# Kernel tuning notes

Measured on AMD Instinct MI355X. Metric: run time of the kernel, lower is better.

## Reference

```python
import jax, jax.numpy as jnp
import numpy as np

NC = 80          # num classes
REG_MAX = 16     # DFL bins
STRIDES = (8, 16, 32)
FEAT_HW = ((80, 80), (40, 40), (20, 20))
MAX_DET = 100
CONF_THRES = 0.25
IOU_THRES = 0.45
PRE_TOPK = 1000  # pre-NMS candidate count (EfficientNMS-style preselection)


def setup_inputs() -> dict:
    key = jax.random.key(0)
    k1, k2, k3 = jax.random.split(key, 3)
    B = 32
    no = 4 * REG_MAX + NC  # 144
    return {
        "p3": jax.random.normal(k1, (B, no, 80, 80), dtype=jnp.float32),
        "p4": jax.random.normal(k2, (B, no, 40, 40), dtype=jnp.float32),
        "p5": jax.random.normal(k3, (B, no, 20, 20), dtype=jnp.float32),
    }


def _make_anchors():
    # grid_cell_offset = 0.5, matching ultralytics make_anchors
    pts, strs = [], []
    for (h, w), s in zip(FEAT_HW, STRIDES):
        sx = jnp.arange(w, dtype=jnp.float32) + 0.5
        sy = jnp.arange(h, dtype=jnp.float32) + 0.5
        yy, xx = jnp.meshgrid(sy, sx, indexing="ij")
        pts.append(jnp.stack([xx.ravel(), yy.ravel()], axis=-1))  # [h*w, 2]
        strs.append(jnp.full((h * w, 1), float(s), dtype=jnp.float32))
    return jnp.concatenate(pts, 0), jnp.concatenate(strs, 0)  # [A,2], [A,1]


def _pairwise_iou(b):
    # b: [K, 4] xyxy
    area = (b[:, 2] - b[:, 0]) * (b[:, 3] - b[:, 1])
    lt = jnp.maximum(b[:, None, :2], b[None, :, :2])
    rb = jnp.minimum(b[:, None, 2:], b[None, :, 2:])
    wh = jnp.clip(rb - lt, 0.0)
    inter = wh[..., 0] * wh[..., 1]
    return inter / (area[:, None] + area[None, :] - inter + 1e-7)


def _nms_single(bxyxy, conf):
    # Greedy class-agnostic NMS over PRE_TOPK score-sorted boxes.
    K = bxyxy.shape[0]
    iou = _pairwise_iou(bxyxy)  # [K, K]
    idx = jnp.arange(K)

    def step(suppressed, xs):
        i, row = xs
        keep = jnp.logical_and(jnp.logical_not(suppressed[i]), conf[i] > 0.0)
        suppressed = jnp.logical_or(suppressed, keep & (row > IOU_THRES) & (idx > i))
        return suppressed, keep

    _, keeps = jax.lax.scan(step, jnp.zeros(K, dtype=bool), (idx, iou))
    return keeps  # [K] bool


def reference(p3, p4, p5):
    feats = [p3, p4, p5]
    B = p3.shape[0]
    no = 4 * REG_MAX + NC
    # concat across scales: [B, no, A]
    x_cat = jnp.concatenate([f.reshape(B, no, -1) for f in feats], axis=2)
    box, cls = x_cat[:, : 4 * REG_MAX], x_cat[:, 4 * REG_MAX:]

    anchors, strd = _make_anchors()  # [A,2], [A,1]
    A = box.shape[-1]

    # DFL: softmax over reg_max bins, expectation with arange weights
    prob = jax.nn.softmax(box.reshape(B, 4, REG_MAX, A), axis=2)
    dist = jnp.einsum("bkra,r->bka", prob, jnp.arange(REG_MAX, dtype=jnp.float32))

    # dist2bbox (xywh) then scale by stride
    anc = anchors.T  # [2, A]
    lt, rb = dist[:, :2], dist[:, 2:]
    x1y1 = anc - lt
    x2y2 = anc + rb
    dbox = jnp.concatenate([(x1y1 + x2y2) * 0.5, x2y2 - x1y1], axis=1) * strd.T  # [B,4,A]

    boxes = dbox.transpose(0, 2, 1)                       # [B, A, 4] xywh
    scores = jax.nn.sigmoid(cls).transpose(0, 2, 1)       # [B, A, NC] (score_activation=1)

    # class-agnostic: best class per box
    conf = scores.max(-1)                                 # [B, A]
    cls_id = jnp.argmax(scores, -1)                       # [B, A]
    conf_m = jnp.where(conf > CONF_THRES, conf, -1.0)

    topv, topi = jax.lax.top_k(conf_m, PRE_TOPK)          # [B, K]
    bsel = jnp.take_along_axis(boxes, topi[..., None], axis=1)  # [B, K, 4]
    cx, cy, w, h = bsel[..., 0], bsel[..., 1], bsel[..., 2], bsel[..., 3]
    bxyxy = jnp.stack([cx - w * 0.5, cy - h * 0.5, cx + w * 0.5, cy + h * 0.5], -1)

    keeps = jax.vmap(_nms_single)(bxyxy, topv)            # [B, K]
    kept_scores = jnp.where(keeps, topv, -1.0)
    dv, di = jax.lax.top_k(kept_scores, MAX_DET)          # [B, MAX_DET]
    valid = dv > 0.0

    det_scores = jnp.where(valid, dv, 0.0)
    det_boxes = jnp.take_along_axis(bxyxy, di[..., None], axis=1) * valid[..., None]
    sel_cls = jnp.take_along_axis(jnp.take_along_axis(cls_id, topi, 1), di, 1)
    det_classes = jnp.where(valid, sel_cls, 0).astype(jnp.int32)
    num_dets = valid.sum(-1, keepdims=True).astype(jnp.int32)
    return num_dets, det_boxes, det_scores, det_classes
```

## Files before the change

### kernel.cpp

```cpp
#include <hip/hip_runtime.h>
#include <math.h>

#define NCLS 80
#define NA 8400
#define NB 32
#define NO 144
#define PRE_TOPK 1000
#define MAX_DET 100

template<int HW, int WDIM, int S>
__device__ __forceinline__ void decode_blk(
    const float* __restrict__ src, int b, int a0, int aoff,
    float* __restrict__ conf, int* __restrict__ clsid, float* __restrict__ box,
    float* s_tile)
{
    int t = threadIdx.x;
    int w = t >> 6;
    int l = t & 63;

    {
        int ch_base = w * 36;
        int chl = ch_base + (l >> 4);
        int aq = (l & 15) * 4;
        int aqc = a0 + aq; if (aqc > HW - 4) aqc = HW - 4;
        const float* gsrc = src + ((size_t)b * NO) * HW + aqc;
        float4 stg[9];
        #pragma unroll
        for (int i = 0; i < 9; ++i)
            stg[i] = *(const float4*)(gsrc + (size_t)(chl + i * 4) * HW);
        #pragma unroll
        for (int i = 0; i < 9; ++i)
            *(float4*)&s_tile[(chl + i * 4) * 64 + aq] = stg[i];
    }
    __syncthreads();

    float v[16];
    #pragma unroll
    for (int r = 0; r < 16; ++r) v[r] = s_tile[(w * 16 + r) * 64 + l];
    float mm = v[0];
    #pragma unroll
    for (int r = 1; r < 16; ++r) mm = fmaxf(mm, v[r]);
    float sum = 0.f, d = 0.f;
    #pragma unroll
    for (int r = 0; r < 16; ++r) {
        float e = __expf(v[r] - mm);
        sum += e;
        d += e * (float)r;
    }
    d *= 1.0f / sum;

    float c[20];
    #pragma unroll
    for (int cc = 0; cc < 20; ++cc) c[cc] = s_tile[(64 + w * 20 + cc) * 64 + l];
    float m = c[0]; int ii = 0;
    #pragma unroll
    for (int cc = 1; cc < 20; ++cc) if (c[cc] > m) { m = c[cc]; ii = cc; }

    __syncthreads();

    float* s_dfl = s_tile;
    float* s_mx  = s_tile + 320;
    int*   s_id  = (int*)(s_tile + 640);
    s_dfl[l * 5 + w] = d;
    s_mx[l * 5 + w]  = m;
    s_id[l * 5 + w]  = w * 20 + ii;
    __syncthreads();

    if (t < 64 && a0 + t < HW) {
        int pos2 = a0 + t;
        float d0 = s_dfl[t * 5 + 0], d1 = s_dfl[t * 5 + 1];
        float d2 = s_dfl[t * 5 + 2], d3 = s_dfl[t * 5 + 3];
        float bm = s_mx[t * 5 + 0]; int bid = s_id[t * 5 + 0];
        float m1 = s_mx[t * 5 + 1]; if (m1 > bm) { bm = m1; bid = s_id[t * 5 + 1]; }
        float m2 = s_mx[t * 5 + 2]; if (m2 > bm) { bm = m2; bid = s_id[t * 5 + 2]; }
        float m3 = s_mx[t * 5 + 3]; if (m3 > bm) { bm = m3; bid = s_id[t * 5 + 3]; }
        float conf_v = 1.0f / (1.0f + __expf(-bm));

        float ax = (float)(pos2 % WDIM) + 0.5f;
        float ay = (float)(pos2 / WDIM) + 0.5f;
        float x1 = ax - d0, y1 = ay - d1;
        float x2 = ax + d2, y2 = ay + d3;
        float cx = ((x1 + x2) * 0.5f) * (float)S;
        float cy = ((y1 + y2) * 0.5f) * (float)S;
        float ww = (x2 - x1) * (float)S;
        float hh = (y2 - y1) * (float)S;

        size_t gid = (size_t)b * NA + aoff + pos2;
        conf[gid]  = conf_v;
        clsid[gid] = bid;
        *(float4*)(box + gid * 4) = make_float4(cx, cy, ww, hh);
    }
}

__global__ __launch_bounds__(256) void k_decode(
    const float* __restrict__ p3, const float* __restrict__ p4, const float* __restrict__ p5,
    float* __restrict__ conf, int* __restrict__ clsid, float* __restrict__ box)
{
    __shared__ float s_tile[NO * 64];
    int blk = blockIdx.x;
    int b = blk / 132;
    int r = blk - b * 132;
    if (r < 100)       decode_blk<6400, 80, 8>(p3, b, r * 64, 0, conf, clsid, box, s_tile);
    else if (r < 125)  decode_blk<1600, 40, 16>(p4, b, (r - 100) * 64, 6400, conf, clsid, box, s_tile);
    else               decode_blk<400, 20, 32>(p5, b, (r - 125) * 64, 8000, conf, clsid, box, s_tile);
}

__device__ __forceinline__ uint32_t ord_bits(float f) {
    uint32_t u = __float_as_uint(f);
    return (u & 0x80000000u) ? ~u : (u | 0x80000000u);
}

__global__ __launch_bounds__(1024) void k_select(
    const float* __restrict__ conf, const float* __restrict__ box, const int* __restrict__ clsid,
    float* __restrict__ topv, float* __restrict__ bxyxy, int* __restrict__ topcls)
{
    int b = blockIdx.x;
    int t = threadIdx.x;
    int lane = t & 63;

    __shared__ uint32_t ob[NA];
    __shared__ uint32_t hist[256];
    __shared__ uint64_t sbuf[1024];
    __shared__ uint32_t s_prefix;
    __shared__ int s_k;
    __shared__ int s_cnt;

    const float* cf = conf + (size_t)b * NA;
    for (int i = t; i < NA; i += 1024) {
        float c = cf[i];
        float cm = (c > 0.25f) ? c : -1.0f;
        ob[i] = ord_bits(cm);
    }
    if (t == 0) { s_prefix = 0; s_k = PRE_TOPK; s_cnt = 0; }
    sbuf[t] = 0;
    __syncthreads();

    for (int pass = 0; pass < 4; ++pass) {
        int shift = 24 - 8 * pass;
        if (t < 256) hist[t] = 0;
        __syncthreads();
        uint32_t prefix = s_prefix;
        int k = s_k;
        for (int i = t; i < NA; i += 1024) {
            uint32_t key = ob[i];
            bool match = (pass == 0) || (((key ^ prefix) >> (32 - 8 * pass)) == 0);
            uint32_t d = (key >> shift) & 255u;
            if (match) {
                uint64_t m = __ballot(1);
                #pragma unroll
                for (int bb = 0; bb < 8; ++bb) {
                    uint64_t bal = __ballot((d >> bb) & 1u);
                    m &= ((d >> bb) & 1u) ? bal : ~bal;
                }
                if ((m & ((1ull << lane) - 1ull)) == 0ull)
                    atomicAdd(&hist[d], (uint32_t)__popcll(m));
            }
        }
        __syncthreads();
        if (t < 64) {
            uint32_t h0 = hist[4 * t + 0], h1 = hist[4 * t + 1];
            uint32_t h2 = hist[4 * t + 2], h3 = hist[4 * t + 3];
            uint32_t part = h0 + h1 + h2 + h3;
            uint32_t s = part;
            #pragma unroll
            for (int off = 1; off < 64; off <<= 1) {
                uint32_t v = __shfl_down(s, off);
                if (t + off < 64) s += v;
            }
            uint32_t cb3 = s - part;
            uint32_t cb2 = cb3 + h3;
            uint32_t cb1 = cb2 + h2;
            uint32_t cb0 = cb1 + h1;
            uint32_t ku = (uint32_t)k;
            if (cb3 < ku && ku <= cb3 + h3) { s_k = k - (int)cb3; s_prefix = prefix | ((uint32_t)(4 * t + 3) << shift); }
            if (cb2 < ku && ku <= cb2 + h2) { s_k = k - (int)cb2; s_prefix = prefix | ((uint32_t)(4 * t + 2) << shift); }
            if (cb1 < ku && ku <= cb1 + h1) { s_k = k - (int)cb1; s_prefix = prefix | ((uint32_t)(4 * t + 1) << shift); }
            if (cb0 < ku && ku <= cb0 + h0) { s_k = k - (int)cb0; s_prefix = prefix | ((uint32_t)(4 * t + 0) << shift); }
        }
        __syncthreads();
    }

    uint32_t kstar = s_prefix;
    for (int i = t; i < NA; i += 1024) {
        uint32_t key = ob[i];
        if (key >= kstar) {
            int p = atomicAdd(&s_cnt, 1);
            if (p < 1024) sbuf[p] = ((uint64_t)key << 14) | (uint64_t)(16383 - i);
        }
    }
    __syncthreads();

    uint64_t v = sbuf[t];
    for (int k = 2; k <= 1024; k <<= 1) {
        for (int j = k >> 1; j > 0; j >>= 1) {
            uint64_t o;
            if (j >= 64) {
                sbuf[t] = v;
                __syncthreads();
                o = sbuf[t ^ j];
                __syncthreads();
            } else {
                o = __shfl_xor((unsigned long long)v, j);
            }
            bool desc  = ((t & k) == 0);
            bool lower = ((t & j) == 0);
            v = (desc == lower) ? (v > o ? v : o) : (v < o ? v : o);
        }
    }

    if (t < PRE_TOPK) {
        uint64_t key = v;
        uint32_t u = (uint32_t)(key >> 14);
        uint32_t fb = (u & 0x80000000u) ? (u ^ 0x80000000u) : ~u;
        float val = __uint_as_float(fb);
        int idx = 16383 - (int)(key & 16383u);
        size_t g = (size_t)b * NA + idx;
        float4 bx = *(const float4*)(box + g * 4);
        float cx = bx.x, cy = bx.y, w = bx.z, h = bx.w;
        size_t o = (size_t)b * PRE_TOPK + t;
        topv[o] = val;
        *(float4*)(bxyxy + o * 4) = make_float4(cx - w * 0.5f, cy - h * 0.5f,
                                                cx + w * 0.5f, cy + h * 0.5f);
        topcls[o] = clsid[g];
    }
}

__device__ __forceinline__ int bslot(int j) { return j + (j >> 6); }

__global__ __launch_bounds__(256) void k_iou(
    const float* __restrict__ bxyxy, unsigned long long* __restrict__ mask)
{
    __shared__ float4 boxes[PRE_TOPK + 16];
    int b = blockIdx.y;
    int t = threadIdx.x;
    const float4* bp = (const float4*)(bxyxy + (size_t)b * PRE_TOPK * 4);
    for (int i = t; i < PRE_TOPK; i += 256) boxes[bslot(i)] = bp[i];
    __syncthreads();

    int r_local = t >> 4, w = t & 15;
    int row = blockIdx.x * 16 + r_local;
    if (row >= PRE_TOPK) return;

    float4 bi = boxes[bslot(row)];
    float area_i = (bi.z - bi.x) * (bi.w - bi.y);
    unsigned long long bits = 0;
    int j0 = w * 64;
    #pragma unroll 4
    for (int jj = 0; jj < 64; ++jj) {
        int j = j0 + jj;
        if (j >= PRE_TOPK) break;
        if (j <= row) continue;
        float4 bj = boxes[bslot(j)];
        float lx = fmaxf(bi.x, bj.x), ly = fmaxf(bi.y, bj.y);
        float rx = fminf(bi.z, bj.z), ry = fminf(bi.w, bj.w);
        float iw = fmaxf(rx - lx, 0.f), ih = fmaxf(ry - ly, 0.f);
        float inter = iw * ih;
        float area_j = (bj.z - bj.x) * (bj.w - bj.y);
        float iou = inter / (area_i + area_j - inter + 1e-7f);
        if (iou > 0.45f) bits |= (1ull << jj);
    }
    mask[((size_t)b * PRE_TOPK + row) * 16 + w] = bits;
}

__global__ __launch_bounds__(1024) void k_nms(
    const unsigned long long* __restrict__ mask, const float* __restrict__ topv,
    const float* __restrict__ bxyxy, const int* __restrict__ topcls,
    float* __restrict__ out)
{
    int b = blockIdx.x;
    int t = threadIdx.x;

    __shared__ __align__(16) unsigned long long smask[PRE_TOPK * 16];
    __shared__ float sv[PRE_TOPK];
    __shared__ unsigned long long s_valid[16];
    __shared__ int kept[MAX_DET];
    __shared__ int s_cnt;

    for (int i = t; i < PRE_TOPK; i += 1024) sv[i] = topv[(size_t)b * PRE_TOPK + i];
    {
        const ulonglong2* src = (const ulonglong2*)(mask + (size_t)b * PRE_TOPK * 16);
        ulonglong2* dst = (ulonglong2*)smask;
        for (int i = t; i < PRE_TOPK * 8; i += 1024) dst[i] = src[i];
    }
    __syncthreads();

    {
        bool pred = (t < PRE_TOPK) && (sv[t] > 0.0f);
        unsigned long long bal = __ballot(pred);
        if ((t & 63) == 0) s_valid[t >> 6] = bal;
    }
    __syncthreads();

    if (t < 64) {
        int w = t;
        unsigned long long supp = 0;
        unsigned long long valid = (w < 16) ? s_valid[w] : 0ull;
        int base = w * 64;
        int cur = -1;
        int cnt = 0;
        while (cnt < MAX_DET) {
            unsigned long long gt;
            if (cur < base)            gt = ~0ull;
            else if (cur - base >= 63) gt = 0ull;
            else                       gt = (~0ull) << (cur - base + 1);
            unsigned long long cand = valid & ~supp & gt;
            int idx = cand ? (base + __builtin_ctzll(cand)) : 0x7FFFFFFF;
            #pragma unroll
            for (int off = 8; off >= 1; off >>= 1) {
                int o = __shfl_xor(idx, off);
                idx = (o < idx) ? o : idx;
            }
            int nxt = __shfl(idx, 0);
            if (nxt == 0x7FFFFFFF) break;
            if (t == 0) kept[cnt] = nxt;
            ++cnt;
            if (w < 16) supp |= smask[nxt * 16 + w];
            cur = nxt;
        }
        if (t == 0) s_cnt = cnt;
    }
    __syncthreads();

    int cnt = s_cnt; if (cnt > MAX_DET) cnt = MAX_DET;
    if (t == 0) out[b] = (float)cnt;
    if (t < MAX_DET) {
        bool valid = t < cnt;
        float bx0 = 0.f, bx1 = 0.f, bx2 = 0.f, bx3 = 0.f, sc = 0.f, cl = 0.f;
        if (valid) {
            int p = kept[t];
            size_t o = (size_t)b * PRE_TOPK + p;
            float4 bb = *(const float4*)(bxyxy + o * 4);
            bx0 = bb.x; bx1 = bb.y; bx2 = bb.z; bx3 = bb.w;
            sc = sv[p];
            cl = (float)topcls[o];
        }
        size_t db = 32 + ((size_t)b * MAX_DET + t) * 4;
        out[db + 0] = bx0; out[db + 1] = bx1; out[db + 2] = bx2; out[db + 3] = bx3;
        out[32 + 12800 + (size_t)b * MAX_DET + t] = sc;
        out[32 + 16000 + (size_t)b * MAX_DET + t] = cl;
    }
}

extern "C" void kernel_launch(void* const* d_in, const int* in_sizes, int n_in,
                              void* d_out, int out_size, void* d_ws, size_t ws_size,
                              hipStream_t stream)
{
    const float* p3 = (const float*)d_in[0];
    const float* p4 = (const float*)d_in[1];
    const float* p5 = (const float*)d_in[2];
    float* out = (float*)d_out;

    char* ws = (char*)d_ws;
    size_t off_mask = 0;
    size_t off_conf = off_mask + (size_t)NB * PRE_TOPK * 16 * 8;
    size_t off_cls  = off_conf + (size_t)NB * NA * 4;
    size_t off_box  = off_cls  + (size_t)NB * NA * 4;
    size_t off_topv = off_box  + (size_t)NB * NA * 4 * 4;
    size_t off_topc = off_topv + (size_t)NB * PRE_TOPK * 4;
    size_t off_bx   = off_topc + (size_t)NB * PRE_TOPK * 4;

    unsigned long long* mask = (unsigned long long*)(ws + off_mask);
    float* conf   = (float*)(ws + off_conf);
    int*   clsid  = (int*)(ws + off_cls);
    float* box    = (float*)(ws + off_box);
    float* topv   = (float*)(ws + off_topv);
    int*   topcls = (int*)(ws + off_topc);
    float* bxyxy  = (float*)(ws + off_bx);

    k_decode<<<NB * 132, 256, 0, stream>>>(p3, p4, p5, conf, clsid, box);
    k_select<<<NB, 1024, 0, stream>>>(conf, box, clsid, topv, bxyxy, topcls);
    k_iou<<<dim3((PRE_TOPK + 15) / 16, NB), 256, 0, stream>>>(bxyxy, mask);
    k_nms<<<NB, 1024, 0, stream>>>(mask, topv, bxyxy, topcls, out);
}
```

Measured before the change: 136.4 us.

## Merge select, IoU and NMS kernels into one cooperative kernel with grid syncs

Replaces the three post-decode kernels with a single cooperative kernel of 128 blocks. It runs top-k selection on 32 blocks, the IoU mask on all blocks via a strided task loop, and greedy NMS on 32 blocks, separated by grid-wide syncs. The goal is to remove two kernel launch gaps. In exchange, the IoU stage runs on 128 blocks instead of about 2000 small ones, each block reloads boxes per task, and grid syncs add their own cost.

```diff
diff --git a/kernel.cpp b/kernel.cpp
--- a/kernel.cpp
+++ b/kernel.cpp
@@ -1,5 +1,8 @@
 #include <hip/hip_runtime.h>
+#include <hip/hip_cooperative_groups.h>
 #include <math.h>
+
+namespace cg = cooperative_groups;
 
 #define NCLS 80
 #define NA 8400
@@ -7,6 +10,7 @@
 #define NO 144
 #define PRE_TOPK 1000
 #define MAX_DET 100
+#define POST_GRID 128
 
 template<int HW, int WDIM, int S>
 __device__ __forceinline__ void decode_blk(
@@ -105,239 +109,247 @@
     else               decode_blk<400, 20, 32>(p5, b, (r - 125) * 64, 8000, conf, clsid, box, s_tile);
 }
 
+#define SMX 132416
+
+__device__ __forceinline__ int bslot(int j) { return j + (j >> 6); }
+
 __device__ __forceinline__ uint32_t ord_bits(float f) {
     uint32_t u = __float_as_uint(f);
     return (u & 0x80000000u) ? ~u : (u | 0x80000000u);
 }
 
-__global__ __launch_bounds__(1024) void k_select(
+__global__ __launch_bounds__(1024) void k_post(
     const float* __restrict__ conf, const float* __restrict__ box, const int* __restrict__ clsid,
-    float* __restrict__ topv, float* __restrict__ bxyxy, int* __restrict__ topcls)
+    float* __restrict__ topv, float* __restrict__ bxyxy, int* __restrict__ topcls,
+    unsigned long long* __restrict__ mask, float* __restrict__ out)
 {
-    int b = blockIdx.x;
+    cg::grid_group grid = cg::this_grid();
     int t = threadIdx.x;
     int lane = t & 63;
 
-    __shared__ uint32_t ob[NA];
-    __shared__ uint32_t hist[256];
-    __shared__ uint64_t sbuf[1024];
+    __shared__ __align__(16) char smem[SMX];
     __shared__ uint32_t s_prefix;
     __shared__ int s_k;
-    __shared__ int s_cnt;
-
-    const float* cf = conf + (size_t)b * NA;
-    for (int i = t; i < NA; i += 1024) {
-        float c = cf[i];
-        float cm = (c > 0.25f) ? c : -1.0f;
-        ob[i] = ord_bits(cm);
-    }
-    if (t == 0) { s_prefix = 0; s_k = PRE_TOPK; s_cnt = 0; }
-    sbuf[t] = 0;
-    __syncthreads();
-
-    for (int pass = 0; pass < 4; ++pass) {
-        int shift = 24 - 8 * pass;
-        if (t < 256) hist[t] = 0;
-        __syncthreads();
-        uint32_t prefix = s_prefix;
-        int k = s_k;
+    __shared__ int s_cmp_cnt;
+    __shared__ unsigned long long s_valid[16];
+    __shared__ int s_nms_cnt;
+
+    if (blockIdx.x < NB) {
+        int b = blockIdx.x;
+        uint32_t* ob   = (uint32_t*)smem;
+        uint32_t* hist = (uint32_t*)(smem + 33600);
+        uint64_t* sbuf = (uint64_t*)(smem + 34624);
+
+        const float* cf = conf + (size_t)b * NA;
+        for (int i = t; i < NA; i += 1024) {
+            float c = cf[i];
+            float cm = (c > 0.25f) ? c : -1.0f;
+            ob[i] = ord_bits(cm);
+        }
+        if (t == 0) { s_prefix = 0; s_k = PRE_TOPK; s_cmp_cnt = 0; }
+        sbuf[t] = 0;
+        __syncthreads();
+
+        for (int pass = 0; pass < 4; ++pass) {
+            int shift = 24 - 8 * pass;
+            if (t < 256) hist[t] = 0;
+            __syncthreads();
+            uint32_t prefix = s_prefix;
+            int k = s_k;
+            for (int i = t; i < NA; i += 1024) {
+                uint32_t key = ob[i];
+                bool match = (pass == 0) || (((key ^ prefix) >> (32 - 8 * pass)) == 0);
+                uint32_t d = (key >> shift) & 255u;
+                if (match) {
+                    uint64_t m = __ballot(1);
+                    #pragma unroll
+                    for (int bb = 0; bb < 8; ++bb) {
+                        uint64_t bal = __ballot((d >> bb) & 1u);
+                        m &= ((d >> bb) & 1u) ? bal : ~bal;
+                    }
+                    if ((m & ((1ull << lane) - 1ull)) == 0ull)
+                        atomicAdd(&hist[d], (uint32_t)__popcll(m));
+                }
+            }
+            __syncthreads();
+            if (t < 64) {
+                uint32_t h0 = hist[4 * t + 0], h1 = hist[4 * t + 1];
+                uint32_t h2 = hist[4 * t + 2], h3 = hist[4 * t + 3];
+                uint32_t part = h0 + h1 + h2 + h3;
+                uint32_t s = part;
+                #pragma unroll
+                for (int off = 1; off < 64; off <<= 1) {
+                    uint32_t v = __shfl_down(s, off);
+                    if (t + off < 64) s += v;
+                }
+                uint32_t cb3 = s - part;
+                uint32_t cb2 = cb3 + h3;
+                uint32_t cb1 = cb2 + h2;
+                uint32_t cb0 = cb1 + h1;
+                uint32_t ku = (uint32_t)k;
+                if (cb3 < ku && ku <= cb3 + h3) { s_k = k - (int)cb3; s_prefix = prefix | ((uint32_t)(4 * t + 3) << shift); }
+                if (cb2 < ku && ku <= cb2 + h2) { s_k = k - (int)cb2; s_prefix = prefix | ((uint32_t)(4 * t + 2) << shift); }
+                if (cb1 < ku && ku <= cb1 + h1) { s_k = k - (int)cb1; s_prefix = prefix | ((uint32_t)(4 * t + 1) << shift); }
+                if (cb0 < ku && ku <= cb0 + h0) { s_k = k - (int)cb0; s_prefix = prefix | ((uint32_t)(4 * t + 0) << shift); }
+            }
+            __syncthreads();
+        }
+
+        uint32_t kstar = s_prefix;
         for (int i = t; i < NA; i += 1024) {
             uint32_t key = ob[i];
-            bool match = (pass == 0) || (((key ^ prefix) >> (32 - 8 * pass)) == 0);
-            uint32_t d = (key >> shift) & 255u;
-            if (match) {
-                uint64_t m = __ballot(1);
+            if (key >= kstar) {
+                int p = atomicAdd(&s_cmp_cnt, 1);
+                if (p < 1024) sbuf[p] = ((uint64_t)key << 14) | (uint64_t)(16383 - i);
+            }
+        }
+        __syncthreads();
+
+        uint64_t v = sbuf[t];
+        for (int k = 2; k <= 1024; k <<= 1) {
+            for (int j = k >> 1; j > 0; j >>= 1) {
+                uint64_t o;
+                if (j >= 64) {
+                    sbuf[t] = v;
+                    __syncthreads();
+                    o = sbuf[t ^ j];
+                    __syncthreads();
+                } else {
+                    o = __shfl_xor((unsigned long long)v, j);
+                }
+                bool desc  = ((t & k) == 0);
+                bool lower = ((t & j) == 0);
+                v = (desc == lower) ? (v > o ? v : o) : (v < o ? v : o);
+            }
+        }
+
+        if (t < PRE_TOPK) {
+            uint64_t key = v;
+            uint32_t u = (uint32_t)(key >> 14);
+            uint32_t fb = (u & 0x80000000u) ? (u ^ 0x80000000u) : ~u;
+            float val = __uint_as_float(fb);
+            int idx = 16383 - (int)(key & 16383u);
+            size_t g = (size_t)b * NA + idx;
+            float4 bx = *(const float4*)(box + g * 4);
+            float cx = bx.x, cy = bx.y, w = bx.z, h = bx.w;
+            size_t o = (size_t)b * PRE_TOPK + t;
+            topv[o] = val;
+            *(float4*)(bxyxy + o * 4) = make_float4(cx - w * 0.5f, cy - h * 0.5f,
+                                                    cx + w * 0.5f, cy + h * 0.5f);
+            topcls[o] = clsid[g];
+        }
+    }
+
+    __threadfence();
+    grid.sync();
+
+    {
+        float4* boxes = (float4*)smem;
+        for (int task = blockIdx.x; task < NB * 16; task += gridDim.x) {
+            int b = task >> 4, ti = task & 15;
+            __syncthreads();
+            if (t < PRE_TOPK)
+                boxes[bslot(t)] = ((const float4*)(bxyxy + (size_t)b * PRE_TOPK * 4))[t];
+            __syncthreads();
+
+            int rl = t >> 4, w = t & 15;
+            int row = ti * 64 + rl;
+            if (row < PRE_TOPK) {
+                float4 bi = boxes[bslot(row)];
+                float area_i = (bi.z - bi.x) * (bi.w - bi.y);
+                unsigned long long bits = 0;
+                int j0 = w * 64;
+                #pragma unroll 4
+                for (int jj = 0; jj < 64; ++jj) {
+                    int j = j0 + jj;
+                    if (j >= PRE_TOPK) break;
+                    if (j <= row) continue;
+                    float4 bj = boxes[bslot(j)];
+                    float lx = fmaxf(bi.x, bj.x), ly = fmaxf(bi.y, bj.y);
+                    float rx = fminf(bi.z, bj.z), ry = fminf(bi.w, bj.w);
+                    float iw = fmaxf(rx - lx, 0.f), ih = fmaxf(ry - ly, 0.f);
+                    float inter = iw * ih;
+                    float area_j = (bj.z - bj.x) * (bj.w - bj.y);
+                    float iou = inter / (area_i + area_j - inter + 1e-7f);
+                    if (iou > 0.45f) bits |= (1ull << jj);
+                }
+                mask[((size_t)b * PRE_TOPK + row) * 16 + w] = bits;
+            }
+        }
+    }
+
+    __threadfence();
+    grid.sync();
+
+    if (blockIdx.x < NB) {
+        int b = blockIdx.x;
+        unsigned long long* smask = (unsigned long long*)smem;
+        float* sv = (float*)(smem + 128000);
+        int* kept = (int*)(smem + 132000);
+
+        for (int i = t; i < PRE_TOPK; i += 1024) sv[i] = topv[(size_t)b * PRE_TOPK + i];
+        {
+            const ulonglong2* src = (const ulonglong2*)(mask + (size_t)b * PRE_TOPK * 16);
+            ulonglong2* dst = (ulonglong2*)smask;
+            for (int i = t; i < PRE_TOPK * 8; i += 1024) dst[i] = src[i];
+        }
+        __syncthreads();
+
+        {
+            bool pred = (t < PRE_TOPK) && (sv[t] > 0.0f);
+            unsigned long long bal = __ballot(pred);
+            if ((t & 63) == 0) s_valid[t >> 6] = bal;
+        }
+        __syncthreads();
+
+        if (t < 64) {
+            int w = t;
+            unsigned long long supp = 0;
+            unsigned long long valid = (w < 16) ? s_valid[w] : 0ull;
+            int base = w * 64;
+            int cur = -1;
+            int cnt = 0;
+            while (cnt < MAX_DET) {
+                unsigned long long gt;
+                if (cur < base)            gt = ~0ull;
+                else if (cur - base >= 63) gt = 0ull;
+                else                       gt = (~0ull) << (cur - base + 1);
+                unsigned long long cand = valid & ~supp & gt;
+                int idx = cand ? (base + __builtin_ctzll(cand)) : 0x7FFFFFFF;
                 #pragma unroll
-                for (int bb = 0; bb < 8; ++bb) {
-                    uint64_t bal = __ballot((d >> bb) & 1u);
-                    m &= ((d >> bb) & 1u) ? bal : ~bal;
-                }
-                if ((m & ((1ull << lane) - 1ull)) == 0ull)
-                    atomicAdd(&hist[d], (uint32_t)__popcll(m));
-            }
-        }
-        __syncthreads();
-        if (t < 64) {
-            uint32_t h0 = hist[4 * t + 0], h1 = hist[4 * t + 1];
-            uint32_t h2 = hist[4 * t + 2], h3 = hist[4 * t + 3];
-            uint32_t part = h0 + h1 + h2 + h3;
-            uint32_t s = part;
-            #pragma unroll
-            for (int off = 1; off < 64; off <<= 1) {
-                uint32_t v = __shfl_down(s, off);
-                if (t + off < 64) s += v;
-            }
-            uint32_t cb3 = s - part;
-            uint32_t cb2 = cb3 + h3;
-            uint32_t cb1 = cb2 + h2;
-            uint32_t cb0 = cb1 + h1;
-            uint32_t ku = (uint32_t)k;
-            if (cb3 < ku && ku <= cb3 + h3) { s_k = k - (int)cb3; s_prefix = prefix | ((uint32_t)(4 * t + 3) << shift); }
-            if (cb2 < ku && ku <= cb2 + h2) { s_k = k - (int)cb2; s_prefix = prefix | ((uint32_t)(4 * t + 2) << shift); }
-            if (cb1 < ku && ku <= cb1 + h1) { s_k = k - (int)cb1; s_prefix = prefix | ((uint32_t)(4 * t + 1) << shift); }
-            if (cb0 < ku && ku <= cb0 + h0) { s_k = k - (int)cb0; s_prefix = prefix | ((uint32_t)(4 * t + 0) << shift); }
-        }
-        __syncthreads();
-    }
-
-    uint32_t kstar = s_prefix;
-    for (int i = t; i < NA; i += 1024) {
-        uint32_t key = ob[i];
-        if (key >= kstar) {
-            int p = atomicAdd(&s_cnt, 1);
-            if (p < 1024) sbuf[p] = ((uint64_t)key << 14) | (uint64_t)(16383 - i);
-        }
-    }
-    __syncthreads();
-
-    uint64_t v = sbuf[t];
-    for (int k = 2; k <= 1024; k <<= 1) {
-        for (int j = k >> 1; j > 0; j >>= 1) {
-            uint64_t o;
-            if (j >= 64) {
-                sbuf[t] = v;
-                __syncthreads();
-                o = sbuf[t ^ j];
-                __syncthreads();
-            } else {
-                o = __shfl_xor((unsigned long long)v, j);
-            }
-            bool desc  = ((t & k) == 0);
-            bool lower = ((t & j) == 0);
-            v = (desc == lower) ? (v > o ? v : o) : (v < o ? v : o);
-        }
-    }
-
-    if (t < PRE_TOPK) {
-        uint64_t key = v;
-        uint32_t u = (uint32_t)(key >> 14);
-        uint32_t fb = (u & 0x80000000u) ? (u ^ 0x80000000u) : ~u;
-        float val = __uint_as_float(fb);
-        int idx = 16383 - (int)(key & 16383u);
-        size_t g = (size_t)b * NA + idx;
-        float4 bx = *(const float4*)(box + g * 4);
-        float cx = bx.x, cy = bx.y, w = bx.z, h = bx.w;
-        size_t o = (size_t)b * PRE_TOPK + t;
-        topv[o] = val;
-        *(float4*)(bxyxy + o * 4) = make_float4(cx - w * 0.5f, cy - h * 0.5f,
-                                                cx + w * 0.5f, cy + h * 0.5f);
-        topcls[o] = clsid[g];
-    }
-}
-
-__device__ __forceinline__ int bslot(int j) { return j + (j >> 6); }
-
-__global__ __launch_bounds__(256) void k_iou(
-    const float* __restrict__ bxyxy, unsigned long long* __restrict__ mask)
-{
-    __shared__ float4 boxes[PRE_TOPK + 16];
-    int b = blockIdx.y;
-    int t = threadIdx.x;
-    const float4* bp = (const float4*)(bxyxy + (size_t)b * PRE_TOPK * 4);
-    for (int i = t; i < PRE_TOPK; i += 256) boxes[bslot(i)] = bp[i];
-    __syncthreads();
-
-    int r_local = t >> 4, w = t & 15;
-    int row = blockIdx.x * 16 + r_local;
-    if (row >= PRE_TOPK) return;
-
-    float4 bi = boxes[bslot(row)];
-    float area_i = (bi.z - bi.x) * (bi.w - bi.y);
-    unsigned long long bits = 0;
-    int j0 = w * 64;
-    #pragma unroll 4
-    for (int jj = 0; jj < 64; ++jj) {
-        int j = j0 + jj;
-        if (j >= PRE_TOPK) break;
-        if (j <= row) continue;
-        float4 bj = boxes[bslot(j)];
-        float lx = fmaxf(bi.x, bj.x), ly = fmaxf(bi.y, bj.y);
-        float rx = fminf(bi.z, bj.z), ry = fminf(bi.w, bj.w);
-        float iw = fmaxf(rx - lx, 0.f), ih = fmaxf(ry - ly, 0.f);
-        float inter = iw * ih;
-        float area_j = (bj.z - bj.x) * (bj.w - bj.y);
-        float iou = inter / (area_i + area_j - inter + 1e-7f);
-        if (iou > 0.45f) bits |= (1ull << jj);
-    }
-    mask[((size_t)b * PRE_TOPK + row) * 16 + w] = bits;
-}
-
-__global__ __launch_bounds__(1024) void k_nms(
-    const unsigned long long* __restrict__ mask, const float* __restrict__ topv,
-    const float* __restrict__ bxyxy, const int* __restrict__ topcls,
-    float* __restrict__ out)
-{
-    int b = blockIdx.x;
-    int t = threadIdx.x;
-
-    __shared__ __align__(16) unsigned long long smask[PRE_TOPK * 16];
-    __shared__ float sv[PRE_TOPK];
-    __shared__ unsigned long long s_valid[16];
-    __shared__ int kept[MAX_DET];
-    __shared__ int s_cnt;
-
-    for (int i = t; i < PRE_TOPK; i += 1024) sv[i] = topv[(size_t)b * PRE_TOPK + i];
-    {
-        const ulonglong2* src = (const ulonglong2*)(mask + (size_t)b * PRE_TOPK * 16);
-        ulonglong2* dst = (ulonglong2*)smask;
-        for (int i = t; i < PRE_TOPK * 8; i += 1024) dst[i] = src[i];
-    }
-    __syncthreads();
-
-    {
-        bool pred = (t < PRE_TOPK) && (sv[t] > 0.0f);
-        unsigned long long bal = __ballot(pred);
-        if ((t & 63) == 0) s_valid[t >> 6] = bal;
-    }
-    __syncthreads();
-
-    if (t < 64) {
-        int w = t;
-        unsigned long long supp = 0;
-        unsigned long long valid = (w < 16) ? s_valid[w] : 0ull;
-        int base = w * 64;
-        int cur = -1;
-        int cnt = 0;
-        while (cnt < MAX_DET) {
-            unsigned long long gt;
-            if (cur < base)            gt = ~0ull;
-            else if (cur - base >= 63) gt = 0ull;
-            else                       gt = (~0ull) << (cur - base + 1);
-            unsigned long long cand = valid & ~supp & gt;
-            int idx = cand ? (base + __builtin_ctzll(cand)) : 0x7FFFFFFF;
-            #pragma unroll
-            for (int off = 8; off >= 1; off >>= 1) {
-                int o = __shfl_xor(idx, off);
-                idx = (o < idx) ? o : idx;
-            }
-            int nxt = __shfl(idx, 0);
-            if (nxt == 0x7FFFFFFF) break;
-            if (t == 0) kept[cnt] = nxt;
-            ++cnt;
-            if (w < 16) supp |= smask[nxt * 16 + w];
-            cur = nxt;
-        }
-        if (t == 0) s_cnt = cnt;
-    }
-    __syncthreads();
-
-    int cnt = s_cnt; if (cnt > MAX_DET) cnt = MAX_DET;
-    if (t == 0) out[b] = (float)cnt;
-    if (t < MAX_DET) {
-        bool valid = t < cnt;
-        float bx0 = 0.f, bx1 = 0.f, bx2 = 0.f, bx3 = 0.f, sc = 0.f, cl = 0.f;
-        if (valid) {
-            int p = kept[t];
-            size_t o = (size_t)b * PRE_TOPK + p;
-            float4 bb = *(const float4*)(bxyxy + o * 4);
-            bx0 = bb.x; bx1 = bb.y; bx2 = bb.z; bx3 = bb.w;
-            sc = sv[p];
-            cl = (float)topcls[o];
-        }
-        size_t db = 32 + ((size_t)b * MAX_DET + t) * 4;
-        out[db + 0] = bx0; out[db + 1] = bx1; out[db + 2] = bx2; out[db + 3] = bx3;
-        out[32 + 12800 + (size_t)b * MAX_DET + t] = sc;
-        out[32 + 16000 + (size_t)b * MAX_DET + t] = cl;
+                for (int off = 8; off >= 1; off >>= 1) {
+                    int o = __shfl_xor(idx, off);
+                    idx = (o < idx) ? o : idx;
+                }
+                int nxt = __shfl(idx, 0);
+                if (nxt == 0x7FFFFFFF) break;
+                if (t == 0) kept[cnt] = nxt;
+                ++cnt;
+                if (w < 16) supp |= smask[nxt * 16 + w];
+                cur = nxt;
+            }
+            if (t == 0) s_nms_cnt = cnt;
+        }
+        __syncthreads();
+
+        int cnt = s_nms_cnt; if (cnt > MAX_DET) cnt = MAX_DET;
+        if (t == 0) out[b] = (float)cnt;
+        if (t < MAX_DET) {
+            bool valid = t < cnt;
+            float bx0 = 0.f, bx1 = 0.f, bx2 = 0.f, bx3 = 0.f, sc = 0.f, cl = 0.f;
+            if (valid) {
+                int p = kept[t];
+                size_t o = (size_t)b * PRE_TOPK + p;
+                float4 bb = *(const float4*)(bxyxy + o * 4);
+                bx0 = bb.x; bx1 = bb.y; bx2 = bb.z; bx3 = bb.w;
+                sc = sv[p];
+                cl = (float)topcls[o];
+            }
+            size_t db = 32 + ((size_t)b * MAX_DET + t) * 4;
+            out[db + 0] = bx0; out[db + 1] = bx1; out[db + 2] = bx2; out[db + 3] = bx3;
+            out[32 + 12800 + (size_t)b * MAX_DET + t] = sc;
+            out[32 + 16000 + (size_t)b * MAX_DET + t] = cl;
+        }
     }
 }
 
@@ -368,7 +380,10 @@
     float* bxyxy  = (float*)(ws + off_bx);
 
     k_decode<<<NB * 132, 256, 0, stream>>>(p3, p4, p5, conf, clsid, box);
-    k_select<<<NB, 1024, 0, stream>>>(conf, box, clsid, topv, bxyxy, topcls);
-    k_iou<<<dim3((PRE_TOPK + 15) / 16, NB), 256, 0, stream>>>(bxyxy, mask);
-    k_nms<<<NB, 1024, 0, stream>>>(mask, topv, bxyxy, topcls, out);
-}
+
+    void* args[] = { (void*)&conf, (void*)&box, (void*)&clsid,
+                     (void*)&topv, (void*)&bxyxy, (void*)&topcls,
+                     (void*)&mask, (void*)&out };
+    hipLaunchCooperativeKernel((const void*)k_post, dim3(POST_GRID), dim3(1024),
+                               args, 0, stream);
+}
```

Result: slower. 264.7 us (+94.1%).
